# Kernel tuning notes

Hardware: AMD Instinct MI355X
Metric: run time of the kernel (lower is better)

The kernel has to match this reference:

```python
import jax, jax.numpy as jnp
import numpy as np

B, T, D = 4, 2048, 1024
H, HS = 16, 64  # n_head, head_size


def setup_inputs() -> dict:
    key = jax.random.key(0)
    ks = jax.random.split(key, 6)
    s_in = 1.0 / np.sqrt(D)
    s_out = 1.0 / np.sqrt(H * HS)
    x = jax.random.normal(ks[0], (B, T, D), dtype=jnp.float32)
    Wq = jax.random.uniform(ks[1], (H, D, HS), jnp.float32, -s_in, s_in)
    Wk = jax.random.uniform(ks[2], (H, D, HS), jnp.float32, -s_in, s_in)
    Wv = jax.random.uniform(ks[3], (H, D, HS), jnp.float32, -s_in, s_in)
    Wo = jax.random.uniform(ks[4], (H * HS, D), jnp.float32, -s_out, s_out)
    bo = jax.random.uniform(ks[5], (D,), jnp.float32, -s_out, s_out)
    return {"x": x, "Wq": Wq, "Wk": Wk, "Wv": Wv, "Wo": Wo, "bo": bo}


def reference(x, Wq, Wk, Wv, Wo, bo):
    # per-head projections, batched across heads: [B,T,D] x [H,D,HS] -> [B,H,T,HS]
    q = jnp.einsum("btd,hde->bhte", x, Wq)
    k = jnp.einsum("btd,hde->bhte", x, Wk)
    v = jnp.einsum("btd,hde->bhte", x, Wv)
    scale = HS ** -0.5
    scores = jnp.einsum("bhqe,bhke->bhqk", q, k) * scale  # [B,H,T,T]
    causal = jnp.tril(jnp.ones((T, T), dtype=bool))
    scores = jnp.where(causal, scores, jnp.float32(-jnp.inf))
    attn = jax.nn.softmax(scores, axis=-1)
    out = jnp.einsum("bhqk,bhke->bhqe", attn, v)  # [B,H,T,HS]
    out = out.transpose(0, 2, 1, 3).reshape(B, T, H * HS)  # concat heads
    return out @ Wo + bo
```

## Files before the change

### kernel.cpp

```cpp
#include <hip/hip_runtime.h>

typedef __attribute__((ext_vector_type(8))) short short8v;
typedef __attribute__((ext_vector_type(4))) short short4v;
typedef __attribute__((ext_vector_type(4))) float floatx4;

namespace {
constexpr int Bn = 4, Tn = 2048, Dn = 1024, Hn = 16, HSn = 64;
}

__device__ __forceinline__ short f2bf(float f) {
  unsigned u = __builtin_bit_cast(unsigned, f);
  u += 0x7fffu + ((u >> 16) & 1u);
  return (short)(u >> 16);
}

typedef const __attribute__((address_space(1))) unsigned int guint_t;
typedef __attribute__((address_space(3))) unsigned int luint_t;

__device__ __forceinline__ void gload16(const void* g, void* l) {
  __builtin_amdgcn_global_load_lds((guint_t*)g, (luint_t*)l, 16, 0, 0);
}

__device__ __forceinline__ short8v rd8(const char* base, int row, int kel) {
  return *(const short8v*)(base + row * 128 + ((kel * 2) ^ ((row & 7) << 4)));
}

__global__ __launch_bounds__(256) void cvt_x_k(const float* __restrict__ x, short* __restrict__ xb) {
  const size_t i = ((size_t)blockIdx.x * 256 + threadIdx.x) * 8;
  const float4 a = *(const float4*)(x + i);
  const float4 b = *(const float4*)(x + i + 4);
  short8v o;
  o[0] = f2bf(a.x); o[1] = f2bf(a.y); o[2] = f2bf(a.z); o[3] = f2bf(a.w);
  o[4] = f2bf(b.x); o[5] = f2bf(b.y); o[6] = f2bf(b.z); o[7] = f2bf(b.w);
  *(short8v*)(xb + i) = o;
}

__global__ __launch_bounds__(256) void tr_wqkv_k(const float* __restrict__ Wq, const float* __restrict__ Wk,
                                                 const float* __restrict__ Wv, short* __restrict__ wt) {
  const int ph = blockIdx.x;
  const int p = ph >> 4, h = ph & 15;
  const int dt = blockIdx.y;
  const float* W = p == 0 ? Wq : p == 1 ? Wk : Wv;
  __shared__ float T[64][65];
  const int t = threadIdx.x;
  const int rr = t >> 2, c0 = (t & 3) * 4;
  const float* src = W + (size_t)h * (Dn * HSn) + (size_t)(dt * 64 + rr) * HSn;
  #pragma unroll
  for (int q = 0; q < 4; ++q) {
    const float4 v = *(const float4*)(src + c0 + q * 16);
    T[rr][c0 + q * 16 + 0] = v.x; T[rr][c0 + q * 16 + 1] = v.y;
    T[rr][c0 + q * 16 + 2] = v.z; T[rr][c0 + q * 16 + 3] = v.w;
  }
  __syncthreads();
  short* dst = wt + ((size_t)p * 1024 + h * 64 + rr) * 1024 + dt * 64;
  #pragma unroll
  for (int q = 0; q < 4; ++q) {
    const int dl = c0 + q * 16;
    short4v ov = {f2bf(T[dl + 0][rr]), f2bf(T[dl + 1][rr]),
                  f2bf(T[dl + 2][rr]), f2bf(T[dl + 3][rr])};
    *(short4v*)(dst + dl) = ov;
  }
}

__global__ __launch_bounds__(256) void tr_wo_k(const float* __restrict__ Wo, short* __restrict__ wot) {
  const int ktile = blockIdx.x, ntile = blockIdx.y;
  __shared__ float T[64][65];
  const int t = threadIdx.x;
  const int rr = t >> 2, c0 = (t & 3) * 4;
  const float* src = Wo + (size_t)(ktile * 64 + rr) * Dn + ntile * 64;
  #pragma unroll
  for (int q = 0; q < 4; ++q) {
    const float4 v = *(const float4*)(src + c0 + q * 16);
    T[rr][c0 + q * 16 + 0] = v.x; T[rr][c0 + q * 16 + 1] = v.y;
    T[rr][c0 + q * 16 + 2] = v.z; T[rr][c0 + q * 16 + 3] = v.w;
  }
  __syncthreads();
  short* dst = wot + (size_t)(ntile * 64 + rr) * 1024 + ktile * 64;
  #pragma unroll
  for (int q = 0; q < 4; ++q) {
    const int dl = c0 + q * 16;
    short4v ov = {f2bf(T[dl + 0][rr]), f2bf(T[dl + 1][rr]),
                  f2bf(T[dl + 2][rr]), f2bf(T[dl + 3][rr])};
    *(short4v*)(dst + dl) = ov;
  }
}

__device__ __forceinline__ void gemm_mainloop(const char* gA, const char* gB, char* As, char* Bs,
                                              floatx4 acc[4][4]) {
  const int tid = threadIdx.x;
  const int wv = tid >> 6, ln = tid & 63;
  const int wr = wv >> 1, wc = wv & 1;
  const int lr = ln >> 3, lg = ln & 7;
  const int fr = ln & 15, kq = ln >> 4;
  for (int kt = 0; kt < 16; ++kt) {
    __syncthreads();
    #pragma unroll
    for (int c = 0; c < 4; ++c) {
      const int r = wv * 32 + c * 8 + lr;
      const int sw = (lg * 16) ^ ((r & 7) * 16);
      gload16(gA + (size_t)r * 2048 + kt * 128 + sw, As + (wv * 32 + c * 8) * 128);
      gload16(gB + (size_t)r * 2048 + kt * 128 + sw, Bs + (wv * 32 + c * 8) * 128);
    }
    __syncthreads();
    #pragma unroll
    for (int kb = 0; kb < 2; ++kb) {
      const int k0 = kb * 32 + kq * 8;
      short8v af[4], bfr[4];
      #pragma unroll
      for (int i = 0; i < 4; ++i) af[i] = rd8(As, wr * 64 + i * 16 + fr, k0);
      #pragma unroll
      for (int j = 0; j < 4; ++j) bfr[j] = rd8(Bs, wc * 64 + j * 16 + fr, k0);
      #pragma unroll
      for (int i = 0; i < 4; ++i)
        #pragma unroll
        for (int j = 0; j < 4; ++j)
          acc[i][j] = __builtin_amdgcn_mfma_f32_16x16x32_bf16(af[i], bfr[j], acc[i][j], 0, 0, 0);
    }
  }
}

__global__ __launch_bounds__(256) void gemm_qkv_k(const short* __restrict__ xb, const short* __restrict__ wt,
                                                  short* __restrict__ qb, short* __restrict__ kb,
                                                  short* __restrict__ vb) {
  __shared__ __align__(16) char As[16384];
  __shared__ __align__(16) char Bs[16384];
  const int m0 = blockIdx.x * 128, n0 = blockIdx.y * 128;
  floatx4 acc[4][4];
  #pragma unroll
  for (int i = 0; i < 4; ++i)
    #pragma unroll
    for (int j = 0; j < 4; ++j) acc[i][j] = floatx4{0.f, 0.f, 0.f, 0.f};
  gemm_mainloop((const char*)xb + (size_t)m0 * 2048, (const char*)wt + (size_t)n0 * 2048, As, Bs, acc);

  const int tid = threadIdx.x, wv = tid >> 6, ln = tid & 63;
  const int wr = wv >> 1, wc = wv & 1;
  const int proj = n0 >> 10;
  const int b = m0 >> 11;
  const int rb_ = (ln >> 4) * 4, fc = ln & 15;
  if (proj < 2) {
    short* dst = proj == 0 ? qb : kb;
    const float sc = proj == 0 ? 0.18033688011112042f : 1.0f;
    #pragma unroll
    for (int i = 0; i < 4; ++i) {
      const int m = m0 + wr * 64 + i * 16 + rb_;
      #pragma unroll
      for (int j = 0; j < 4; ++j) {
        const int n = n0 + wc * 64 + j * 16 + fc;
        const int h = (n >> 6) & 15, e = n & 63;
        short* dp = dst + ((size_t)(b * 16 + h) * Tn + (m & 2047)) * 64 + e;
        #pragma unroll
        for (int r = 0; r < 4; ++r) dp[(size_t)r * 64] = f2bf(acc[i][j][r] * sc);
      }
    }
  } else {
    #pragma unroll
    for (int i = 0; i < 4; ++i) {
      const int m = m0 + wr * 64 + i * 16 + rb_;
      const int t0 = m & 2047;
      #pragma unroll
      for (int j = 0; j < 4; ++j) {
        const int n = n0 + wc * 64 + j * 16 + fc;
        const int h = (n >> 6) & 15, e = n & 63;
        short4v ov = {f2bf(acc[i][j][0]), f2bf(acc[i][j][1]),
                      f2bf(acc[i][j][2]), f2bf(acc[i][j][3])};
        *(short4v*)(vb + ((size_t)(b * 16 + h) * 64 + e) * Tn + t0) = ov;
      }
    }
  }
}

__global__ __launch_bounds__(256, 3) void attn_k(const short* __restrict__ qg, const short* __restrict__ kg,
                                                 const short* __restrict__ vg, short* __restrict__ og) {
  __shared__ __align__(16) char Qs[16384];
  __shared__ __align__(16) char Ks[16384];
  __shared__ __align__(16) char Vs[16384];
  char* Ps = Qs;
  const int qt = gridDim.y - 1 - blockIdx.y;
  const int bh = blockIdx.x;
  const int tid = threadIdx.x, wv = tid >> 6, ln = tid & 63;
  const int lr = ln >> 3, lg = ln & 7;
  const int fr = ln & 15, kq = ln >> 4;
  const char* qbase = (const char*)qg + (size_t)bh * Tn * 128;
  const char* kbase = (const char*)kg + (size_t)bh * Tn * 128;
  const char* vbase = (const char*)vg + (size_t)bh * Tn * 128;

  #pragma unroll
  for (int c = 0; c < 4; ++c) {
    const int r = c * 32 + wv * 8 + lr;
    const int sw = (lg * 16) ^ ((r & 7) * 16);
    gload16(qbase + (size_t)(qt * 128 + r) * 128 + sw, Qs + (c * 32 + wv * 8) * 128);
  }
  #pragma unroll
  for (int c = 0; c < 2; ++c) {
    const int r = c * 32 + wv * 8 + lr;
    const int sw = (lg * 16) ^ ((r & 7) * 16);
    gload16(kbase + (size_t)r * 128 + sw, Ks + (c * 32 + wv * 8) * 128);
    gload16(vbase + (size_t)r * 4096 + sw, Vs + (c * 32 + wv * 8) * 128);
  }
  __syncthreads();

  short8v qf[2][2];
  #pragma unroll
  for (int c = 0; c < 2; ++c)
    #pragma unroll
    for (int kb = 0; kb < 2; ++kb)
      qf[c][kb] = rd8(Qs, wv * 32 + c * 16 + fr, kb * 32 + kq * 8);

  floatx4 ot[4][2];
  #pragma unroll
  for (int f = 0; f < 4; ++f) { ot[f][0] = floatx4{0.f,0.f,0.f,0.f}; ot[f][1] = floatx4{0.f,0.f,0.f,0.f}; }
  float m_i[2] = {-1e30f, -1e30f}, l_i[2] = {0.f, 0.f};

  const int nkt = 2 * qt + 2;
  const int q0w = qt * 128 + wv * 32;
  for (int kt = 0; kt < nkt; ++kt) {
    const int cur = kt & 1;
    if (kt + 1 < nkt) {
      #pragma unroll
      for (int c = 0; c < 2; ++c) {
        const int r = c * 32 + wv * 8 + lr;
        const int sw = (lg * 16) ^ ((r & 7) * 16);
        gload16(kbase + (size_t)((kt + 1) * 64 + r) * 128 + sw,
                Ks + (cur ^ 1) * 8192 + (c * 32 + wv * 8) * 128);
        gload16(vbase + (size_t)r * 4096 + (size_t)(kt + 1) * 128 + sw,
                Vs + (cur ^ 1) * 8192 + (c * 32 + wv * 8) * 128);
      }
    }
    if (kt * 64 <= q0w + 31) {
      const char* Ksc = Ks + cur * 8192;
      const char* Vsc = Vs + cur * 8192;
      floatx4 st[2][4];
      #pragma unroll
      for (int f = 0; f < 4; ++f) { st[0][f] = floatx4{0.f,0.f,0.f,0.f}; st[1][f] = floatx4{0.f,0.f,0.f,0.f}; }
      #pragma unroll
      for (int kb = 0; kb < 2; ++kb) {
        const int e0 = kb * 32 + kq * 8;
        #pragma unroll
        for (int f = 0; f < 4; ++f) {
          const short8v kf = rd8(Ksc, f * 16 + fr, e0);
          st[0][f] = __builtin_amdgcn_mfma_f32_16x16x32_bf16(kf, qf[0][kb], st[0][f], 0, 0, 0);
          st[1][f] = __builtin_amdgcn_mfma_f32_16x16x32_bf16(kf, qf[1][kb], st[1][f], 0, 0, 0);
        }
      }
      if (kt * 64 + 63 > q0w) {
        #pragma unroll
        for (int c = 0; c < 2; ++c) {
          const int q = q0w + c * 16 + fr;
          #pragma unroll
          for (int f = 0; f < 4; ++f)
            #pragma unroll
            for (int r = 0; r < 4; ++r)
              if (kt * 64 + f * 16 + kq * 4 + r > q) st[c][f][r] = -3.0e38f;
        }
      }
      float al[2];
      #pragma unroll
      for (int c = 0; c < 2; ++c) {
        float mx = st[c][0][0];
        #pragma unroll
        for (int f = 0; f < 4; ++f)
          #pragma unroll
          for (int r = 0; r < 4; ++r) mx = fmaxf(mx, st[c][f][r]);
        mx = fmaxf(mx, __shfl_xor(mx, 16, 64));
        mx = fmaxf(mx, __shfl_xor(mx, 32, 64));
        const float mn = fmaxf(m_i[c], mx);
        al[c] = exp2f(m_i[c] - mn);
        m_i[c] = mn;
        float sum = 0.f;
        const int prow = wv * 32 + c * 16 + fr;
        #pragma unroll
        for (int f = 0; f < 4; ++f) {
          const float p0 = exp2f(st[c][f][0] - mn);
          const float p1 = exp2f(st[c][f][1] - mn);
          const float p2 = exp2f(st[c][f][2] - mn);
          const float p3 = exp2f(st[c][f][3] - mn);
          sum += (p0 + p1) + (p2 + p3);
          short4v pv = {f2bf(p0), f2bf(p1), f2bf(p2), f2bf(p3)};
          *(short4v*)(Ps + prow * 128 + ((f * 32 + kq * 8) ^ ((prow & 7) * 16))) = pv;
        }
        sum += __shfl_xor(sum, 16, 64);
        sum += __shfl_xor(sum, 32, 64);
        l_i[c] = l_i[c] * al[c] + sum;
      }
      #pragma unroll
      for (int f = 0; f < 4; ++f) { ot[f][0] *= al[0]; ot[f][1] *= al[1]; }
      #pragma unroll
      for (int kb = 0; kb < 2; ++kb) {
        const int v0 = kb * 32 + kq * 8;
        const short8v pb0 = rd8(Ps, wv * 32 + fr, v0);
        const short8v pb1 = rd8(Ps, wv * 32 + 16 + fr, v0);
        #pragma unroll
        for (int f = 0; f < 4; ++f) {
          const short8v vf = rd8(Vsc, f * 16 + fr, v0);
          ot[f][0] = __builtin_amdgcn_mfma_f32_16x16x32_bf16(vf, pb0, ot[f][0], 0, 0, 0);
          ot[f][1] = __builtin_amdgcn_mfma_f32_16x16x32_bf16(vf, pb1, ot[f][1], 0, 0, 0);
        }
      }
    }
    __syncthreads();
  }

  const int b = bh >> 4, h = bh & 15;
  #pragma unroll
  for (int c = 0; c < 2; ++c) {
    const float inv = 1.0f / l_i[c];
    const size_t t = (size_t)(b * Tn + qt * 128 + wv * 32 + c * 16 + fr);
    #pragma unroll
    for (int f = 0; f < 4; ++f) {
      short4v o4 = {f2bf(ot[f][c][0] * inv), f2bf(ot[f][c][1] * inv),
                    f2bf(ot[f][c][2] * inv), f2bf(ot[f][c][3] * inv)};
      *(short4v*)(og + t * 1024 + h * 64 + f * 16 + kq * 4) = o4;
    }
  }
}

__global__ __launch_bounds__(256) void gemm_out_k(const short* __restrict__ ao, const short* __restrict__ wot,
                                                  const float* __restrict__ bo, float* __restrict__ out) {
  __shared__ __align__(16) char As[16384];
  __shared__ __align__(16) char Bs[16384];
  const int m0 = blockIdx.x * 128, n0 = blockIdx.y * 128;
  floatx4 acc[4][4];
  #pragma unroll
  for (int i = 0; i < 4; ++i)
    #pragma unroll
    for (int j = 0; j < 4; ++j) acc[i][j] = floatx4{0.f, 0.f, 0.f, 0.f};
  gemm_mainloop((const char*)ao + (size_t)m0 * 2048, (const char*)wot + (size_t)n0 * 2048, As, Bs, acc);

  const int tid = threadIdx.x, wv = tid >> 6, ln = tid & 63;
  const int wr = wv >> 1, wc = wv & 1;
  const int rb_ = (ln >> 4) * 4, fc = ln & 15;
  #pragma unroll
  for (int i = 0; i < 4; ++i) {
    const int m = m0 + wr * 64 + i * 16 + rb_;
    #pragma unroll
    for (int j = 0; j < 4; ++j) {
      const int n = n0 + wc * 64 + j * 16 + fc;
      const float bias = bo[n];
      #pragma unroll
      for (int r = 0; r < 4; ++r) out[(size_t)(m + r) * Dn + n] = acc[i][j][r] + bias;
    }
  }
}

extern "C" void kernel_launch(void* const* d_in, const int* in_sizes, int n_in,
                              void* d_out, int out_size, void* d_ws, size_t ws_size,
                              hipStream_t stream) {
  const float* x  = (const float*)d_in[0];
  const float* Wq = (const float*)d_in[1];
  const float* Wk = (const float*)d_in[2];
  const float* Wv = (const float*)d_in[3];
  const float* Wo = (const float*)d_in[4];
  const float* bo = (const float*)d_in[5];
  float* out = (float*)d_out;

  char* ws = (char*)d_ws;
  short* xb  = (short*)(ws);
  short* wt  = (short*)(ws + (16u << 20));
  short* wot = (short*)(ws + (22u << 20));
  short* qb  = (short*)(ws + (24u << 20));
  short* kb  = (short*)(ws + (40u << 20));
  short* vb  = (short*)(ws + (56u << 20));
  short* ao  = (short*)(ws + (72u << 20));

  cvt_x_k<<<4096, 256, 0, stream>>>(x, xb);
  tr_wqkv_k<<<dim3(48, 16), 256, 0, stream>>>(Wq, Wk, Wv, wt);
  tr_wo_k<<<dim3(16, 16), 256, 0, stream>>>(Wo, wot);
  gemm_qkv_k<<<dim3(64, 24), 256, 0, stream>>>(xb, wt, qb, kb, vb);
  attn_k<<<dim3(64, 16), 256, 0, stream>>>(qb, kb, vb, ao);
  gemm_out_k<<<dim3(64, 8), 256, 0, stream>>>(ao, wot, bo, out);
}
```

Measured before the change: 186.3 us.

## Load V fragments directly to registers, lazily rescale softmax, remap GEMM blocks for XCD locality

The attention kernel stops staging V in LDS and instead loads V fragments straight from global memory into registers for each key tile, freeing 16KB of LDS and dropping the occupancy hint. Online-softmax rescaling is skipped when the new max stays within 8 (log2 units) of the running max, trading exact max tracking for fewer multiplies. bf16 conversions now use the hardware packed-convert instruction instead of manual rounding. Both GEMM kernels remap the flat block index so consecutive blocks scheduled on the same XCD share tiles in L2. The direct global V loads risk exposed latency, since they are no longer prefetched a tile ahead.

```diff
diff --git a/kernel.cpp b/kernel.cpp
--- a/kernel.cpp
+++ b/kernel.cpp
@@ -12,6 +12,12 @@
   unsigned u = __builtin_bit_cast(unsigned, f);
   u += 0x7fffu + ((u >> 16) & 1u);
   return (short)(u >> 16);
+}
+
+__device__ __forceinline__ unsigned pkbf2(float lo, float hi) {
+  unsigned r;
+  asm("v_cvt_pk_bf16_f32 %0, %1, %2" : "=v"(r) : "v"(lo), "v"(hi));
+  return r;
 }
 
 typedef const __attribute__((address_space(1))) unsigned int guint_t;
@@ -124,7 +130,9 @@
                                                   short* __restrict__ vb) {
   __shared__ __align__(16) char As[16384];
   __shared__ __align__(16) char Bs[16384];
-  const int m0 = blockIdx.x * 128, n0 = blockIdx.y * 128;
+  int flat = blockIdx.y * 64 + blockIdx.x;
+  flat = (flat & 7) * 192 + (flat >> 3);
+  const int m0 = (flat & 63) * 128, n0 = (flat >> 6) * 128;
   floatx4 acc[4][4];
   #pragma unroll
   for (int i = 0; i < 4; ++i)
@@ -169,11 +177,10 @@
   }
 }
 
-__global__ __launch_bounds__(256, 3) void attn_k(const short* __restrict__ qg, const short* __restrict__ kg,
-                                                 const short* __restrict__ vg, short* __restrict__ og) {
+__global__ __launch_bounds__(256) void attn_k(const short* __restrict__ qg, const short* __restrict__ kg,
+                                              const short* __restrict__ vg, short* __restrict__ og) {
   __shared__ __align__(16) char Qs[16384];
   __shared__ __align__(16) char Ks[16384];
-  __shared__ __align__(16) char Vs[16384];
   char* Ps = Qs;
   const int qt = gridDim.y - 1 - blockIdx.y;
   const int bh = blockIdx.x;
@@ -195,7 +202,6 @@
     const int r = c * 32 + wv * 8 + lr;
     const int sw = (lg * 16) ^ ((r & 7) * 16);
     gload16(kbase + (size_t)r * 128 + sw, Ks + (c * 32 + wv * 8) * 128);
-    gload16(vbase + (size_t)r * 4096 + sw, Vs + (c * 32 + wv * 8) * 128);
   }
   __syncthreads();
 
@@ -222,13 +228,10 @@
         const int sw = (lg * 16) ^ ((r & 7) * 16);
         gload16(kbase + (size_t)((kt + 1) * 64 + r) * 128 + sw,
                 Ks + (cur ^ 1) * 8192 + (c * 32 + wv * 8) * 128);
-        gload16(vbase + (size_t)r * 4096 + (size_t)(kt + 1) * 128 + sw,
-                Vs + (cur ^ 1) * 8192 + (c * 32 + wv * 8) * 128);
       }
     }
     if (kt * 64 <= q0w + 31) {
       const char* Ksc = Ks + cur * 8192;
-      const char* Vsc = Vs + cur * 8192;
       floatx4 st[2][4];
       #pragma unroll
       for (int f = 0; f < 4; ++f) { st[0][f] = floatx4{0.f,0.f,0.f,0.f}; st[1][f] = floatx4{0.f,0.f,0.f,0.f}; }
@@ -242,6 +245,13 @@
           st[1][f] = __builtin_amdgcn_mfma_f32_16x16x32_bf16(kf, qf[1][kb], st[1][f], 0, 0, 0);
         }
       }
+      short8v vfr[2][4];
+      #pragma unroll
+      for (int kb = 0; kb < 2; ++kb)
+        #pragma unroll
+        for (int f = 0; f < 4; ++f)
+          vfr[kb][f] = *(const short8v*)(vbase + (size_t)(f * 16 + fr) * 4096 +
+                                         (size_t)kt * 128 + (kb * 32 + kq * 8) * 2);
       if (kt * 64 + 63 > q0w) {
         #pragma unroll
         for (int c = 0; c < 2; ++c) {
@@ -253,37 +263,48 @@
               if (kt * 64 + f * 16 + kq * 4 + r > q) st[c][f][r] = -3.0e38f;
         }
       }
-      float al[2];
+      float mx[2];
       #pragma unroll
       for (int c = 0; c < 2; ++c) {
-        float mx = st[c][0][0];
-        #pragma unroll
-        for (int f = 0; f < 4; ++f)
+        float t0 = fmaxf(fmaxf(st[c][0][0], st[c][0][1]), fmaxf(st[c][0][2], st[c][0][3]));
+        float t1 = fmaxf(fmaxf(st[c][1][0], st[c][1][1]), fmaxf(st[c][1][2], st[c][1][3]));
+        float t2 = fmaxf(fmaxf(st[c][2][0], st[c][2][1]), fmaxf(st[c][2][2], st[c][2][3]));
+        float t3 = fmaxf(fmaxf(st[c][3][0], st[c][3][1]), fmaxf(st[c][3][2], st[c][3][3]));
+        float v = fmaxf(fmaxf(t0, t1), fmaxf(t2, t3));
+        v = fmaxf(v, __shfl_xor(v, 16, 64));
+        v = fmaxf(v, __shfl_xor(v, 32, 64));
+        mx[c] = v;
+      }
+      const bool noresc = __all((mx[0] <= m_i[0] + 8.f) && (mx[1] <= m_i[1] + 8.f));
+      if (!noresc) {
+        #pragma unroll
+        for (int c = 0; c < 2; ++c) {
+          const float mn = fmaxf(m_i[c], mx[c]);
+          const float al = exp2f(m_i[c] - mn);
+          m_i[c] = mn;
+          l_i[c] *= al;
           #pragma unroll
-          for (int r = 0; r < 4; ++r) mx = fmaxf(mx, st[c][f][r]);
-        mx = fmaxf(mx, __shfl_xor(mx, 16, 64));
-        mx = fmaxf(mx, __shfl_xor(mx, 32, 64));
-        const float mn = fmaxf(m_i[c], mx);
-        al[c] = exp2f(m_i[c] - mn);
-        m_i[c] = mn;
+          for (int f = 0; f < 4; ++f) ot[f][c] *= al;
+        }
+      }
+      #pragma unroll
+      for (int c = 0; c < 2; ++c) {
+        const int prow = wv * 32 + c * 16 + fr;
         float sum = 0.f;
-        const int prow = wv * 32 + c * 16 + fr;
         #pragma unroll
         for (int f = 0; f < 4; ++f) {
-          const float p0 = exp2f(st[c][f][0] - mn);
-          const float p1 = exp2f(st[c][f][1] - mn);
-          const float p2 = exp2f(st[c][f][2] - mn);
-          const float p3 = exp2f(st[c][f][3] - mn);
+          const float p0 = exp2f(st[c][f][0] - m_i[c]);
+          const float p1 = exp2f(st[c][f][1] - m_i[c]);
+          const float p2 = exp2f(st[c][f][2] - m_i[c]);
+          const float p3 = exp2f(st[c][f][3] - m_i[c]);
           sum += (p0 + p1) + (p2 + p3);
-          short4v pv = {f2bf(p0), f2bf(p1), f2bf(p2), f2bf(p3)};
-          *(short4v*)(Ps + prow * 128 + ((f * 32 + kq * 8) ^ ((prow & 7) * 16))) = pv;
+          uint2 pv = {pkbf2(p0, p1), pkbf2(p2, p3)};
+          *(uint2*)(Ps + prow * 128 + ((f * 32 + kq * 8) ^ ((prow & 7) * 16))) = pv;
         }
         sum += __shfl_xor(sum, 16, 64);
         sum += __shfl_xor(sum, 32, 64);
-        l_i[c] = l_i[c] * al[c] + sum;
-      }
-      #pragma unroll
-      for (int f = 0; f < 4; ++f) { ot[f][0] *= al[0]; ot[f][1] *= al[1]; }
+        l_i[c] += sum;
+      }
       #pragma unroll
       for (int kb = 0; kb < 2; ++kb) {
         const int v0 = kb * 32 + kq * 8;
@@ -291,9 +312,8 @@
         const short8v pb1 = rd8(Ps, wv * 32 + 16 + fr, v0);
         #pragma unroll
         for (int f = 0; f < 4; ++f) {
-          const short8v vf = rd8(Vsc, f * 16 + fr, v0);
-          ot[f][0] = __builtin_amdgcn_mfma_f32_16x16x32_bf16(vf, pb0, ot[f][0], 0, 0, 0);
-          ot[f][1] = __builtin_amdgcn_mfma_f32_16x16x32_bf16(vf, pb1, ot[f][1], 0, 0, 0);
+          ot[f][0] = __builtin_amdgcn_mfma_f32_16x16x32_bf16(vfr[kb][f], pb0, ot[f][0], 0, 0, 0);
+          ot[f][1] = __builtin_amdgcn_mfma_f32_16x16x32_bf16(vfr[kb][f], pb1, ot[f][1], 0, 0, 0);
         }
       }
     }
@@ -307,9 +327,9 @@
     const size_t t = (size_t)(b * Tn + qt * 128 + wv * 32 + c * 16 + fr);
     #pragma unroll
     for (int f = 0; f < 4; ++f) {
-      short4v o4 = {f2bf(ot[f][c][0] * inv), f2bf(ot[f][c][1] * inv),
-                    f2bf(ot[f][c][2] * inv), f2bf(ot[f][c][3] * inv)};
-      *(short4v*)(og + t * 1024 + h * 64 + f * 16 + kq * 4) = o4;
+      uint2 o4 = {pkbf2(ot[f][c][0] * inv, ot[f][c][1] * inv),
+                  pkbf2(ot[f][c][2] * inv, ot[f][c][3] * inv)};
+      *(uint2*)(og + t * 1024 + h * 64 + f * 16 + kq * 4) = o4;
     }
   }
 }
@@ -318,7 +338,9 @@
                                                   const float* __restrict__ bo, float* __restrict__ out) {
   __shared__ __align__(16) char As[16384];
   __shared__ __align__(16) char Bs[16384];
-  const int m0 = blockIdx.x * 128, n0 = blockIdx.y * 128;
+  int flat = blockIdx.y * 64 + blockIdx.x;
+  flat = (flat & 7) * 64 + (flat >> 3);
+  const int m0 = (flat & 63) * 128, n0 = (flat >> 6) * 128;
   floatx4 acc[4][4];
   #pragma unroll
   for (int i = 0; i < 4; ++i)
```

Result: slower. 210.5 us (+13.0%).
